# Optimization experiments

Hardware: AMD Instinct MI355X
Metric: run time of the kernel (lower is better)

## Reference

```python
import jax, jax.numpy as jnp
import numpy as np

D = 1024
HEADS = 16
HD = D // HEADS


def setup_inputs() -> dict:
    key = jax.random.key(0)
    kx, kqkv, kout = jax.random.split(key, 3)
    x = jax.random.normal(kx, (2, 2048, D), dtype=jnp.float32)
    # torch Linear weight is [out, in]; store same layout
    W_qkv = jax.random.normal(kqkv, (3 * D, D), dtype=jnp.float32) * (D ** -0.5)
    W_out = jax.random.normal(kout, (D, D), dtype=jnp.float32) * (D ** -0.5)
    return {"x": x, "W_qkv": W_qkv, "W_out": W_out}


def reference(x, W_qkv, W_out):
    B, T, _ = x.shape
    scale = HD ** -0.5
    qkv = jnp.einsum('btd,ed->bte', x, W_qkv)            # [B,T,3D]
    qkv = qkv.reshape(B, T, 3, HEADS, HD)
    q = jnp.transpose(qkv[:, :, 0], (0, 2, 1, 3))        # [B,H,T,hd]
    k = jnp.transpose(qkv[:, :, 1], (0, 2, 1, 3))
    v = jnp.transpose(qkv[:, :, 2], (0, 2, 1, 3))
    attn = jnp.einsum('bhqd,bhkd->bhqk', q, k) * scale   # [B,H,T,T]
    causal = jnp.tril(jnp.ones((T, T), dtype=bool))
    attn = jnp.where(causal, attn, -jnp.inf)
    attn = jax.nn.softmax(attn, axis=-1)
    out = jnp.einsum('bhqk,bhkd->bhqd', attn, v)         # [B,H,T,hd]
    out = jnp.transpose(out, (0, 2, 1, 3)).reshape(B, T, HEADS * HD)
    return jnp.einsum('btd,ed->bte', out, W_out)
```

## Files before the change

### kernel.cpp

```cpp
#include <hip/hip_runtime.h>
#include <cmath>


typedef unsigned short u16;
typedef unsigned int u32;
typedef short short8 __attribute__((ext_vector_type(8)));
typedef float floatx4 __attribute__((ext_vector_type(4)));

#define T_SZ 2048
#define HD_SZ 64
#define QSCALE 0.1803368801111244f

__device__ __forceinline__ u16 f2bf(float f) {
  unsigned u = __float_as_uint(f);
  u += 0x7fffu + ((u >> 16) & 1u);
  return (u16)(u >> 16);
}

__device__ __forceinline__ u32 pack_bf2(float lo, float hi) {
  return __builtin_amdgcn_perm(__float_as_uint(hi), __float_as_uint(lo), 0x07060302u);
}

__device__ __forceinline__ u32 cvtpk(float a, float b) {
  u32 r;
  asm("v_cvt_pk_bf16_f32 %0, %1, %2" : "=v"(r) : "v"(a), "v"(b));
  return r;
}

__device__ __forceinline__ void pl32swap(u32& a, u32& b) {
  asm("v_permlane32_swap_b32 %0, %1" : "+v"(a), "+v"(b));
}
__device__ __forceinline__ void pl16swap(u32& a, u32& b) {
  asm("v_permlane16_swap_b32 %0, %1" : "+v"(a), "+v"(b));
}

__device__ __forceinline__ void gload16(const u16* g, u16* l) {
  __builtin_amdgcn_global_load_lds(
      (const __attribute__((address_space(1))) void*)g,
      (__attribute__((address_space(3))) void*)l, 16, 0, 0);
}

__global__ __launch_bounds__(256) void cast3(const float* __restrict__ a, u16* __restrict__ ao, int na4,
                                             const float* __restrict__ b, u16* __restrict__ bo, int nb4,
                                             const float* __restrict__ c, u16* __restrict__ co, int nc4) {
  int i = blockIdx.x * 256 + threadIdx.x;
  const float* src;
  u16* dst;
  int j;
  if (i < na4) { src = a; dst = ao; j = i; }
  else if (i < na4 + nb4) { src = b; dst = bo; j = i - na4; }
  else { j = i - na4 - nb4; if (j >= nc4) return; src = c; dst = co; }
  float4 f = ((const float4*)src)[j];
  ushort4 o;
  o.x = f2bf(f.x); o.y = f2bf(f.y); o.z = f2bf(f.z); o.w = f2bf(f.w);
  ((ushort4*)dst)[j] = o;
}

__global__ __launch_bounds__(256, 3) void gemm_qkv(const u16* __restrict__ A,
                                                   const u16* __restrict__ Bt,
                                                   u16* __restrict__ Qf,
                                                   u16* __restrict__ Kf,
                                                   u16* __restrict__ Vf) {
  __shared__ u16 SM[2 * 128 * 64];
  u16* As = SM;
  u16* Bs = SM + 128 * 64;
  const int Kdim = 1024;
  const int tid = threadIdx.x;
  const int lane = tid & 63;
  const int wave = tid >> 6;
  const int quad = lane >> 4;
  const int l16 = lane & 15;
  const int wm = wave >> 1, wn = wave & 1;
  const int m0 = blockIdx.y * 128;
  const int n0 = blockIdx.x * 128;

  floatx4 acc[4][4];
#pragma unroll
  for (int i = 0; i < 4; i++)
#pragma unroll
    for (int j = 0; j < 4; j++) acc[i][j] = (floatx4){0.f, 0.f, 0.f, 0.f};

  const int srow = lane >> 3;
  const int scol = ((lane & 7) ^ srow) * 8;
  const u16* gpA[4];
  const u16* gpB[4];
  u16 *lpA[4], *lpB[4];
#pragma unroll
  for (int u = 0; u < 4; u++) {
    const int row = wave * 32 + u * 8 + srow;
    gpA[u] = A + (size_t)(m0 + row) * Kdim + scol;
    gpB[u] = Bt + (size_t)(n0 + row) * Kdim + scol;
    lpA[u] = As + (wave * 32 + u * 8) * 64 + lane * 8;
    lpB[u] = Bs + (wave * 32 + u * 8) * 64 + lane * 8;
  }

  const int fsw = l16 & 7;

  for (int k0 = 0; k0 < Kdim; k0 += 64) {
    __syncthreads();
#pragma unroll
    for (int u = 0; u < 4; u++) {
      gload16(gpA[u] + k0, lpA[u]);
      gload16(gpB[u] + k0, lpB[u]);
    }
    __syncthreads();

#pragma unroll
    for (int h = 0; h < 2; h++) {
      const int seg = ((h * 4 + quad) ^ fsw) * 8;
      short8 af[4], bf[4];
#pragma unroll
      for (int mt = 0; mt < 4; mt++)
        af[mt] = *(const short8*)&As[(wm * 64 + mt * 16 + l16) * 64 + seg];
#pragma unroll
      for (int nt = 0; nt < 4; nt++)
        bf[nt] = *(const short8*)&Bs[(wn * 64 + nt * 16 + l16) * 64 + seg];
#pragma unroll
      for (int mt = 0; mt < 4; mt++)
#pragma unroll
        for (int nt = 0; nt < 4; nt++)
          acc[mt][nt] = __builtin_amdgcn_mfma_f32_16x16x32_bf16(af[mt], bf[nt], acc[mt][nt], 0, 0, 0);
    }
  }

  const int dest = n0 >> 10;
  const int n0w = n0 + wn * 64;
  const int m_abs = m0 + wm * 64;
  const int b = m_abs >> 11;
  const int t0w = m_abs & 2047;
  const int h = (n0w >> 6) & 15;
  const int bh = b * 16 + h;
  u16* dstp = (dest == 0) ? Qf : (dest == 1) ? Kf : Vf;

  auto do_epi = [&](u16* ep) {
    if (dest == 2) {
#pragma unroll
      for (int nt = 0; nt < 4; nt++) {
#pragma unroll
        for (int mt = 0; mt < 4; mt++) {
          uint2 w;
          w.x = (u32)f2bf(acc[mt][nt][0]) | ((u32)f2bf(acc[mt][nt][1]) << 16);
          w.y = (u32)f2bf(acc[mt][nt][2]) | ((u32)f2bf(acc[mt][nt][3]) << 16);
          *(uint2*)&ep[(nt * 16 + l16) * 72 + mt * 16 + quad * 4] = w;
        }
      }
    } else {
      const float sc = (dest == 0) ? QSCALE : 1.0f;
#pragma unroll
      for (int mt = 0; mt < 4; mt++)
#pragma unroll
        for (int nt = 0; nt < 4; nt++)
#pragma unroll
          for (int r = 0; r < 4; r++)
            ep[(mt * 16 + quad * 4 + r) * 72 + nt * 16 + l16] =
                f2bf(acc[mt][nt][r] * sc);
    }
#pragma unroll
    for (int blk = 0; blk < 8; blk++) {
      const int tgd = blk >> 1;
      const int half = blk & 1;
      const short8 v = *(const short8*)&ep[(tgd * 16 + l16) * 72 + half * 32 + quad * 8];
      size_t base;
      if (dest == 0)
        base = ((size_t)(bh * 128 + (t0w >> 4) + tgd) * 2 + half) * 512;
      else
        base = (((size_t)(bh * 32 + (t0w >> 6)) * 4 + tgd) * 2 + half) * 512;
      *(short8*)(dstp + base + lane * 8) = v;
    }
  };

  __syncthreads();
  if (wave < 2) do_epi(&SM[wave * 64 * 72]);
  __syncthreads();
  if (wave >= 2) do_epi(&SM[(wave - 2) * 64 * 72]);
}

__global__ __launch_bounds__(256, 4) void gemm_out(const u16* __restrict__ A,
                                                   const u16* __restrict__ Bt,
                                                   float* __restrict__ Cout) {
  __shared__ u16 As[64 * 64];
  __shared__ u16 Bs[128 * 64];
  const int Kdim = 1024;
  const int tid = threadIdx.x;
  const int lane = tid & 63;
  const int wave = tid >> 6;
  const int quad = lane >> 4;
  const int l16 = lane & 15;
  const int wm = wave >> 1, wn = wave & 1;
  const int m0 = blockIdx.y * 64;
  const int n0 = blockIdx.x * 128;

  floatx4 acc[2][4];
#pragma unroll
  for (int i = 0; i < 2; i++)
#pragma unroll
    for (int j = 0; j < 4; j++) acc[i][j] = (floatx4){0.f, 0.f, 0.f, 0.f};

  const int srow = lane >> 3;
  const int scol = ((lane & 7) ^ srow) * 8;
  const u16* gpA[2];
  const u16* gpB[4];
  u16 *lpA[2], *lpB[4];
#pragma unroll
  for (int u = 0; u < 2; u++) {
    const int row = wave * 16 + u * 8 + srow;
    gpA[u] = A + (size_t)(m0 + row) * Kdim + scol;
    lpA[u] = As + (wave * 16 + u * 8) * 64 + lane * 8;
  }
#pragma unroll
  for (int u = 0; u < 4; u++) {
    const int row = wave * 32 + u * 8 + srow;
    gpB[u] = Bt + (size_t)(n0 + row) * Kdim + scol;
    lpB[u] = Bs + (wave * 32 + u * 8) * 64 + lane * 8;
  }

  const int fsw = l16 & 7;

  for (int k0 = 0; k0 < Kdim; k0 += 64) {
    __syncthreads();
#pragma unroll
    for (int u = 0; u < 2; u++) gload16(gpA[u] + k0, lpA[u]);
#pragma unroll
    for (int u = 0; u < 4; u++) gload16(gpB[u] + k0, lpB[u]);
    __syncthreads();

#pragma unroll
    for (int h = 0; h < 2; h++) {
      const int seg = ((h * 4 + quad) ^ fsw) * 8;
      short8 af[2], bf[4];
#pragma unroll
      for (int mt = 0; mt < 2; mt++)
        af[mt] = *(const short8*)&As[(wm * 32 + mt * 16 + l16) * 64 + seg];
#pragma unroll
      for (int nt = 0; nt < 4; nt++)
        bf[nt] = *(const short8*)&Bs[(wn * 64 + nt * 16 + l16) * 64 + seg];
#pragma unroll
      for (int mt = 0; mt < 2; mt++)
#pragma unroll
        for (int nt = 0; nt < 4; nt++)
          acc[mt][nt] = __builtin_amdgcn_mfma_f32_16x16x32_bf16(af[mt], bf[nt], acc[mt][nt], 0, 0, 0);
    }
  }

#pragma unroll
  for (int mt = 0; mt < 2; mt++)
#pragma unroll
    for (int nt = 0; nt < 4; nt++)
#pragma unroll
      for (int r = 0; r < 4; r++) {
        const int m = m0 + wm * 32 + mt * 16 + quad * 4 + r;
        const int n = n0 + wn * 64 + nt * 16 + l16;
        Cout[(size_t)m * 1024 + n] = acc[mt][nt][r];
      }
}

__global__ __launch_bounds__(256, 4) void flash_attn(const u16* __restrict__ Qf,
                                                     const u16* __restrict__ Kf,
                                                     const u16* __restrict__ Vf,
                                                     u16* __restrict__ Og) {
  __shared__ __align__(16) u16 KV[2][16 * 512];
  const int tid = threadIdx.x;
  const int lane = tid & 63, wave = tid >> 6;
  const int quad = lane >> 4, l16 = lane & 15;
  const int bh = blockIdx.x;
  const int by = blockIdx.y;
  const int r = by & 7, qq = by >> 3;
  const int g = (qq == 0) ? r : (qq == 1) ? 15 - r : (qq == 2) ? 16 + r : 31 - r;
  const int b = bh >> 4, h = bh & 15;
  const u16* Qb = Qf + ((size_t)bh << 17);
  const u16* Kb = Kf + ((size_t)bh << 17);
  const u16* Vb = Vf + ((size_t)bh << 17);

  const u16* qp = Qb + ((size_t)(g * 4 + wave)) * 1024 + lane * 8;
  const short8 qf0 = *(const short8*)qp;
  const short8 qf1 = *(const short8*)(qp + 512);

  float l_sum = 0.f;
  floatx4 o_acc[4];
#pragma unroll
  for (int dt = 0; dt < 4; dt++) o_acc[dt] = (floatx4){0.f, 0.f, 0.f, 0.f};

  const u16* gkv[4];
  u16* l0[4];
  u16* l1[4];
#pragma unroll
  for (int i = 0; i < 4; i++) {
    const int c = wave * 4 + i;
    gkv[i] = ((c < 8) ? (Kb + c * 512) : (Vb + (c - 8) * 512)) + lane * 8;
    l0[i] = &KV[0][c * 512] + lane * 8;
    l1[i] = &KV[1][c * 512] + lane * 8;
  }

  auto load_tile = [&](int kt, u16* const* lp) {
#pragma unroll
    for (int i = 0; i < 4; i++) gload16(gkv[i] + (size_t)kt * 4096, lp[i]);
  };

  const floatx4 zero4 = {0.f, 0.f, 0.f, 0.f};

  auto compute = [&](int kt, const u16* Kl) {
    const bool diag = (kt == g);
    short8 ka[4][2];
#pragma unroll
    for (int nt = 0; nt < 4; nt++)
#pragma unroll
      for (int hh = 0; hh < 2; hh++)
        ka[nt][hh] = *(const short8*)&Kl[(nt * 2 + hh) * 512 + lane * 8];
    floatx4 sacc[4];
#pragma unroll
    for (int nt = 0; nt < 4; nt++) {
      if (diag && nt > wave) continue;
      floatx4 s = __builtin_amdgcn_mfma_f32_16x16x32_bf16(ka[nt][0], qf0, zero4, 0, 0, 0);
      sacc[nt] = __builtin_amdgcn_mfma_f32_16x16x32_bf16(ka[nt][1], qf1, s, 0, 0, 0);
    }
    u32 c[4][2];
#pragma unroll
    for (int nt = 0; nt < 4; nt++) {
      float p0 = 0.f, p1 = 0.f, p2 = 0.f, p3 = 0.f;
      if (!(diag && nt > wave)) {
        p0 = exp2f(sacc[nt][0]);
        p1 = exp2f(sacc[nt][1]);
        p2 = exp2f(sacc[nt][2]);
        p3 = exp2f(sacc[nt][3]);
        if (diag && nt == wave) {
          if (quad * 4 + 0 > l16) p0 = 0.f;
          if (quad * 4 + 1 > l16) p1 = 0.f;
          if (quad * 4 + 2 > l16) p2 = 0.f;
          if (quad * 4 + 3 > l16) p3 = 0.f;
        }
        l_sum += (p0 + p1) + (p2 + p3);
      }
      c[nt][0] = cvtpk(p0, p1);
      c[nt][1] = cvtpk(p2, p3);
    }
    pl32swap(c[0][0], c[1][0]); pl16swap(c[0][0], c[1][0]);
    pl32swap(c[0][1], c[1][1]); pl16swap(c[0][1], c[1][1]);
    pl32swap(c[2][0], c[3][0]); pl16swap(c[2][0], c[3][0]);
    pl32swap(c[2][1], c[3][1]); pl16swap(c[2][1], c[3][1]);
    union { u32 w[4]; short8 s8; } P0, P1;
    P0.w[0] = c[0][0]; P0.w[1] = c[0][1]; P0.w[2] = c[1][0]; P0.w[3] = c[1][1];
    P1.w[0] = c[2][0]; P1.w[1] = c[2][1]; P1.w[2] = c[3][0]; P1.w[3] = c[3][1];
    const short8 pf0 = P0.s8;
    const short8 pf1 = P1.s8;
    short8 va[4][2];
#pragma unroll
    for (int dt = 0; dt < 4; dt++)
#pragma unroll
      for (int hh = 0; hh < 2; hh++)
        va[dt][hh] = *(const short8*)&Kl[4096 + (dt * 2 + hh) * 512 + lane * 8];
    const bool skip_hi = diag && (wave < 2);
#pragma unroll
    for (int dt = 0; dt < 4; dt++) {
      o_acc[dt] = __builtin_amdgcn_mfma_f32_16x16x32_bf16(va[dt][0], pf0, o_acc[dt], 0, 0, 0);
      if (!skip_hi)
        o_acc[dt] = __builtin_amdgcn_mfma_f32_16x16x32_bf16(va[dt][1], pf1, o_acc[dt], 0, 0, 0);
    }
  };

  load_tile(0, l0);
  __syncthreads();
  int kt = 0;
  for (;;) {
    if (kt < g) load_tile(kt + 1, l1);
    compute(kt, &KV[0][0]);
    if (++kt > g) break;
    __syncthreads();
    if (kt < g) load_tile(kt + 1, l0);
    compute(kt, &KV[1][0]);
    if (++kt > g) break;
    __syncthreads();
  }

  l_sum += __shfl_xor(l_sum, 16, 64);
  l_sum += __shfl_xor(l_sum, 32, 64);
  const float inv_l = 1.0f / l_sum;
  const int t0 = g * 64 + wave * 16;
  const size_t row = ((size_t)(b * 2048 + t0 + l16) << 10) + h * 64;
#pragma unroll
  for (int dt = 0; dt < 4; dt++) {
    uint2 w;
    w.x = pack_bf2(o_acc[dt][0] * inv_l, o_acc[dt][1] * inv_l);
    w.y = pack_bf2(o_acc[dt][2] * inv_l, o_acc[dt][3] * inv_l);
    *(uint2*)&Og[row + dt * 16 + quad * 4] = w;
  }
}

extern "C" void kernel_launch(void* const* d_in, const int* in_sizes, int n_in,
                              void* d_out, int out_size, void* d_ws, size_t ws_size,
                              hipStream_t stream) {
  const float* x = (const float*)d_in[0];
  const float* Wqkv = (const float*)d_in[1];
  const float* Wout = (const float*)d_in[2];
  float* out = (float*)d_out;

  char* ws = (char*)d_ws;
  u16* xb    = (u16*)(ws + 0);
  u16* wqkvb = (u16*)(ws + 8388608);
  u16* woutb = (u16*)(ws + 14680064);
  u16* Qf    = (u16*)(ws + 16777216);
  u16* Kf    = (u16*)(ws + 25165824);
  u16* Vf    = (u16*)(ws + 33554432);
  u16* attn  = (u16*)(ws + 41943040);

  cast3<<<8192, 256, 0, stream>>>(x, xb, 1048576, Wqkv, wqkvb, 786432,
                                  Wout, woutb, 262144);

  gemm_qkv<<<dim3(24, 32), 256, 0, stream>>>(xb, wqkvb, Qf, Kf, Vf);

  flash_attn<<<dim3(32, 32), 256, 0, stream>>>(Qf, Kf, Vf, attn);

  gemm_out<<<dim3(8, 64), 256, 0, stream>>>(attn, woutb, out);
}
```

Before: 166.1 us.

## Compute softmax row sums via MFMA ones-vector and use raw v_exp in attention

```diff
diff --git a/kernel.cpp b/kernel.cpp
--- a/kernel.cpp
+++ b/kernel.cpp
@@ -32,6 +32,17 @@
 }
 __device__ __forceinline__ void pl16swap(u32& a, u32& b) {
   asm("v_permlane16_swap_b32 %0, %1" : "+v"(a), "+v"(b));
+}
+
+__device__ __forceinline__ void exp4(float s0, float s1, float s2, float s3,
+                                     float& p0, float& p1, float& p2, float& p3) {
+  asm("v_exp_f32 %0, %4\n\t"
+      "v_exp_f32 %1, %5\n\t"
+      "v_exp_f32 %2, %6\n\t"
+      "v_exp_f32 %3, %7\n\t"
+      "s_nop 1"
+      : "=&v"(p0), "=&v"(p1), "=&v"(p2), "=&v"(p3)
+      : "v"(s0), "v"(s1), "v"(s2), "v"(s3));
 }
 
 __device__ __forceinline__ void gload16(const u16* g, u16* l) {
@@ -275,10 +286,14 @@
   const short8 qf0 = *(const short8*)qp;
   const short8 qf1 = *(const short8*)(qp + 512);
 
-  float l_sum = 0.f;
+  floatx4 l_acc = (floatx4){0.f, 0.f, 0.f, 0.f};
   floatx4 o_acc[4];
 #pragma unroll
   for (int dt = 0; dt < 4; dt++) o_acc[dt] = (floatx4){0.f, 0.f, 0.f, 0.f};
+
+  short8 onesf;
+#pragma unroll
+  for (int i = 0; i < 8; i++) onesf[i] = (short)0x3F80;
 
   const u16* gkv[4];
   u16* l0[4];
@@ -307,28 +322,26 @@
       for (int hh = 0; hh < 2; hh++)
         ka[nt][hh] = *(const short8*)&Kl[(nt * 2 + hh) * 512 + lane * 8];
     floatx4 sacc[4];
+    __builtin_amdgcn_s_setprio(1);
 #pragma unroll
     for (int nt = 0; nt < 4; nt++) {
       if (diag && nt > wave) continue;
       floatx4 s = __builtin_amdgcn_mfma_f32_16x16x32_bf16(ka[nt][0], qf0, zero4, 0, 0, 0);
       sacc[nt] = __builtin_amdgcn_mfma_f32_16x16x32_bf16(ka[nt][1], qf1, s, 0, 0, 0);
     }
+    __builtin_amdgcn_s_setprio(0);
     u32 c[4][2];
 #pragma unroll
     for (int nt = 0; nt < 4; nt++) {
       float p0 = 0.f, p1 = 0.f, p2 = 0.f, p3 = 0.f;
       if (!(diag && nt > wave)) {
-        p0 = exp2f(sacc[nt][0]);
-        p1 = exp2f(sacc[nt][1]);
-        p2 = exp2f(sacc[nt][2]);
-        p3 = exp2f(sacc[nt][3]);
+        exp4(sacc[nt][0], sacc[nt][1], sacc[nt][2], sacc[nt][3], p0, p1, p2, p3);
         if (diag && nt == wave) {
           if (quad * 4 + 0 > l16) p0 = 0.f;
           if (quad * 4 + 1 > l16) p1 = 0.f;
           if (quad * 4 + 2 > l16) p2 = 0.f;
           if (quad * 4 + 3 > l16) p3 = 0.f;
         }
-        l_sum += (p0 + p1) + (p2 + p3);
       }
       c[nt][0] = cvtpk(p0, p1);
       c[nt][1] = cvtpk(p2, p3);
@@ -349,12 +362,17 @@
       for (int hh = 0; hh < 2; hh++)
         va[dt][hh] = *(const short8*)&Kl[4096 + (dt * 2 + hh) * 512 + lane * 8];
     const bool skip_hi = diag && (wave < 2);
+    __builtin_amdgcn_s_setprio(1);
+    l_acc = __builtin_amdgcn_mfma_f32_16x16x32_bf16(onesf, pf0, l_acc, 0, 0, 0);
+    if (!skip_hi)
+      l_acc = __builtin_amdgcn_mfma_f32_16x16x32_bf16(onesf, pf1, l_acc, 0, 0, 0);
 #pragma unroll
     for (int dt = 0; dt < 4; dt++) {
       o_acc[dt] = __builtin_amdgcn_mfma_f32_16x16x32_bf16(va[dt][0], pf0, o_acc[dt], 0, 0, 0);
       if (!skip_hi)
         o_acc[dt] = __builtin_amdgcn_mfma_f32_16x16x32_bf16(va[dt][1], pf1, o_acc[dt], 0, 0, 0);
     }
+    __builtin_amdgcn_s_setprio(0);
   };
 
   load_tile(0, l0);
@@ -371,9 +389,7 @@
     __syncthreads();
   }
 
-  l_sum += __shfl_xor(l_sum, 16, 64);
-  l_sum += __shfl_xor(l_sum, 32, 64);
-  const float inv_l = 1.0f / l_sum;
+  const float inv_l = 1.0f / l_acc[0];
   const int t0 = g * 64 + wave * 16;
   const size_t row = ((size_t)(b * 2048 + t0 + l16) << 10) + h * 64;
 #pragma unroll
```

New measurement: 155.7 us. 1.07x faster.
